# Kernel optimization log

Measured on AMD Instinct MI355X. Metric: run time of the kernel, lower is better.

## Reference

```python
import jax, jax.numpy as jnp
import numpy as np

N = 8192   # nodes per modality
D = 128    # hidden_channels
H = 2      # transformer heads
R = 15     # relations in HeteroConv (use_speaker='no')
E = 16384  # edges per relation
L = 2      # num_layers
# relation src/dst node-type ids: 0=audio, 1=text, 2=visual (dict order: a/v/t past, a/v/t future, a/v/t self, then cross)
SRC = np.array([0, 2, 1, 0, 2, 1, 0, 2, 1, 0, 0, 2, 2, 1, 1])
DST = np.array([0, 2, 1, 0, 2, 1, 0, 2, 1, 2, 1, 0, 1, 0, 2])


def setup_inputs() -> dict:
    key = jax.random.key(0)
    ks = jax.random.split(key, 18)
    f = lambda k, sh: jax.random.normal(k, sh, dtype=jnp.float32) * 0.05
    return {
        "x_audio": jax.random.normal(ks[0], (N, D), jnp.float32),
        "x_text": jax.random.normal(ks[1], (N, D), jnp.float32),
        "x_visual": jax.random.normal(ks[2], (N, D), jnp.float32),
        "edge_index": jax.random.randint(ks[3], (R, 2, E), 0, N, jnp.int32),
        "Wrel": f(ks[4], (L, R, D, D)),
        "brel": f(ks[5], (L, R, D)),
        "Wroot": f(ks[6], (L, R, D, D)),
        "Wq": f(ks[7], (D, H * D)), "bq": f(ks[8], (H * D,)),
        "Wk": f(ks[9], (D, H * D)), "bk": f(ks[10], (H * D,)),
        "Wv": f(ks[11], (D, H * D)), "bv": f(ks[12], (H * D,)),
        "Wskip": f(ks[13], (D, D)), "bskip": f(ks[14], (D,)),
        "gamma": jnp.ones((D,), jnp.float32),
        "beta": jnp.zeros((D,), jnp.float32),
    }


def reference(x_audio, x_text, x_visual, edge_index, Wrel, brel, Wroot,
              Wq, bq, Wk, bk, Wv, bv, Wskip, bskip, gamma, beta):
    src_t = jnp.asarray(SRC)
    dst_t = jnp.asarray(DST)
    x = jnp.stack([x_audio, x_text, x_visual])           # [3, N, D]
    src_idx = edge_index[:, 0]                            # [R, E]
    dst_idx = edge_index[:, 1]                            # [R, E]
    rel = jnp.arange(R)

    # --- HeteroConv of 15 GraphConvs (aggr='add' inside, 'mean' over the 5 relations per dst type) ---
    seg = (rel[:, None] * N + dst_idx).reshape(-1)        # per-relation segment ids
    for l in range(L):
        feats = jnp.take_along_axis(x[src_t], src_idx[:, :, None], axis=1)     # [R, E, D]
        msg = jax.ops.segment_sum(feats.reshape(R * E, D), seg,
                                  num_segments=R * N).reshape(R, N, D)          # scatter-add per relation
        out = (jnp.einsum('rnd,rde->rne', msg, Wrel[l]) + brel[l][:, None, :]
               + jnp.einsum('rnd,rde->rne', x[dst_t], Wroot[l]))                # lin_rel(agg) + lin_root(x_dst)
        x = jax.nn.relu(jnp.zeros_like(x).at[dst_t].add(out) / 5.0)            # mean over 5 relations per dst

    # --- hetero_to_homo: concat audio, text, visual (offsets 0, N, 2N) ---
    hx = x.reshape(3 * N, D)
    src_h = (src_t[:, None] * N + src_idx).reshape(-1)    # [R*E]
    dst_h = (dst_t[:, None] * N + dst_idx).reshape(-1)

    # --- TransformerConv (concat=False -> head mean, root skip) ---
    q = (hx @ Wq + bq).reshape(3 * N, H, D)
    k = (hx @ Wk + bk).reshape(3 * N, H, D)
    v = (hx @ Wv + bv).reshape(3 * N, H, D)
    logits = jnp.einsum('ehd,ehd->eh', q[dst_h], k[src_h]) / jnp.sqrt(jnp.float32(D))
    m = jax.ops.segment_max(logits, dst_h, num_segments=3 * N)
    p = jnp.exp(logits - m[dst_h])
    denom = jax.ops.segment_sum(p, dst_h, num_segments=3 * N)
    alpha = p / denom[dst_h]                              # segment softmax over incoming edges
    agg = jax.ops.segment_sum(alpha[:, :, None] * v[src_h], dst_h, num_segments=3 * N)  # [3N, H, D]
    out = agg.mean(axis=1) + hx @ Wskip + bskip

    # --- BatchNorm1d (training-mode batch stats) + leaky_relu ---
    mu = out.mean(axis=0)
    var = ((out - mu) ** 2).mean(axis=0)
    y = (out - mu) / jnp.sqrt(var + 1e-5) * gamma + beta
    y = jax.nn.leaky_relu(y)                              # negative_slope=0.01 (torch default)
    return y.reshape(3, N, D)                             # [audio, text, visual]
```

## Files before the change

### kernel.cpp

```cpp
#include <hip/hip_runtime.h>
#include <hip/hip_bf16.h>

#define NN 8192
#define DD 128
#define HH 2
#define RR 15
#define EE 16384
#define NLAYER 2
#define NMOD 3
#define TN (NMOD*NN)
#define NE (RR*EE)

#define SRC_BITS 0x16818618u
#define DST_BITS 0x21198618u
__device__ __forceinline__ int srcOf(int r) { return (SRC_BITS >> (2 * r)) & 3; }
__device__ __forceinline__ int dstOf(int r) { return (DST_BITS >> (2 * r)) & 3; }

typedef __attribute__((ext_vector_type(8))) short bf16x8;
typedef __attribute__((ext_vector_type(4))) float f32x4;

__device__ __forceinline__ unsigned short f2bf(float v) {
    union { float f; unsigned int u; } x; x.f = v;
    unsigned int r = (x.u + 0x7fffu + ((x.u >> 16) & 1u)) >> 16;
    return (unsigned short)r;
}
__device__ __forceinline__ float bf2f(unsigned int bits16) {
    return __uint_as_float(bits16 << 16);
}
__device__ __forceinline__ void bfu4(uint4 u, float* f) {
    f[0] = bf2f(u.x & 0xffffu); f[1] = bf2f(u.x >> 16);
    f[2] = bf2f(u.y & 0xffffu); f[3] = bf2f(u.y >> 16);
    f[4] = bf2f(u.z & 0xffffu); f[5] = bf2f(u.z >> 16);
    f[6] = bf2f(u.w & 0xffffu); f[7] = bf2f(u.w >> 16);
}

__global__ __launch_bounds__(256) void prep_all(
        const float* __restrict__ Wrel, const float* __restrict__ Wroot,
        const float* __restrict__ brel,
        const float* __restrict__ Wq, const float* __restrict__ Wk,
        const float* __restrict__ Wv, const float* __restrict__ Wskip,
        const float* __restrict__ xa, const float* __restrict__ xt,
        const float* __restrict__ xv,
        unsigned short* __restrict__ WrelT, unsigned short* __restrict__ WsumT,
        float* __restrict__ bsum,
        unsigned short* __restrict__ WqT, unsigned short* __restrict__ WkT,
        unsigned short* __restrict__ WvT, unsigned short* __restrict__ WskipT,
        unsigned short* __restrict__ xb, int* __restrict__ cnt) {
    int y = blockIdx.y;
    int t = blockIdx.x * 256 + threadIdx.x;
    if (y < 30) {
        int k = t >> 7, c = t & 127;
        WrelT[(size_t)y * 16384 + c * 128 + k] = f2bf(Wrel[(size_t)y * 16384 + t]);
    } else if (y < 36) {
        int mat = y - 30, l = mat / 3, m = mat % 3;
        int k = t >> 7, c = t & 127;
        float s = 0.f;
        #pragma unroll
        for (int r = 0; r < RR; r++)
            if (((DST_BITS >> (2 * r)) & 3) == (unsigned)m) s += Wroot[(size_t)(l * RR + r) * 16384 + t];
        WsumT[(size_t)mat * 16384 + c * 128 + k] = f2bf(s);
        if (blockIdx.x == 0 && threadIdx.x < 128) {
            float b = 0.f;
            #pragma unroll
            for (int r = 0; r < RR; r++)
                if (((DST_BITS >> (2 * r)) & 3) == (unsigned)m) b += brel[(l * RR + r) * 128 + threadIdx.x];
            bsum[mat * 128 + threadIdx.x] = b;
        }
    } else if (y < 39) {
        int which = y - 36;
        const float* s = which == 0 ? Wq : which == 1 ? Wk : Wv;
        unsigned short* d = which == 0 ? WqT : which == 1 ? WkT : WvT;
        #pragma unroll
        for (int it = 0; it < 2; it++) {
            int tt = t + it * 16384;
            int k = tt >> 8, c = tt & 255;
            d[c * 128 + k] = f2bf(s[tt]);
        }
    } else if (y == 39) {
        int k = t >> 7, c = t & 127;
        WskipT[c * 128 + k] = f2bf(Wskip[t]);
    } else if (y == 40) {
        for (int i = t; i < TN + 256; i += 16384) cnt[i] = 0;
    } else {
        int m = y - 41;
        const float* s = m == 0 ? xa : m == 1 ? xt : xv;
        unsigned short* d = xb + (size_t)m * NN * DD;
        for (int i = t * 4; i < NN * DD; i += 16384 * 4) {
            float4 v = *(const float4*)(s + i);
            uint2 o;
            o.x = (unsigned)f2bf(v.x) | ((unsigned)f2bf(v.y) << 16);
            o.y = (unsigned)f2bf(v.z) | ((unsigned)f2bf(v.w) << 16);
            *(uint2*)(d + i) = o;
        }
    }
}

__global__ void count_edges(const int* __restrict__ edge, int* __restrict__ cnt) {
    int t = blockIdx.x * 256 + threadIdx.x;
    if (t >= NE) return;
    int r = t >> 14, e = t & (EE - 1);
    int dst = edge[r * 2 * EE + EE + e];
    atomicAdd(&cnt[dstOf(r) * NN + dst], 1);
}

__global__ void scan_kernel(const int* __restrict__ cnt, int* __restrict__ startA,
                            int* __restrict__ cursor) {
    __shared__ int part[1024];
    int t = threadIdx.x;
    int base = t * (TN / 1024);
    int s = 0;
    for (int i = 0; i < TN / 1024; i++) s += cnt[base + i];
    part[t] = s;
    __syncthreads();
    for (int ofs = 1; ofs < 1024; ofs <<= 1) {
        int v = (t >= ofs) ? part[t - ofs] : 0;
        __syncthreads();
        part[t] += v;
        __syncthreads();
    }
    int run = (t == 0) ? 0 : part[t - 1];
    for (int i = 0; i < TN / 1024; i++) {
        startA[base + i] = run;
        cursor[base + i] = run;
        run += cnt[base + i];
    }
    if (t == 1023) startA[TN] = part[1023];
}

__global__ void place_edges(const int* __restrict__ edge, int* __restrict__ cursor,
                            unsigned int* __restrict__ sorted) {
    int t = blockIdx.x * 256 + threadIdx.x;
    if (t >= NE) return;
    int r = t >> 14, e = t & (EE - 1);
    int src = edge[r * 2 * EE + e];
    int dst = edge[r * 2 * EE + EE + e];
    int pos = atomicAdd(&cursor[dstOf(r) * NN + dst], 1);
    sorted[pos] = ((unsigned int)r << 13) | (unsigned int)src;
}

template<int MODE>
__device__ __forceinline__ void gemm_tile(const unsigned short* __restrict__ A,
                                          const unsigned short* __restrict__ BT,
                                          const float* __restrict__ bias,
                                          void* __restrict__ Cout,
                                          int ldc, int colofs, int row0,
                                          unsigned short* lds) {
    unsigned short* Alds = lds;
    unsigned short* Blds = lds + 16384;
    const int tid = threadIdx.x;
    const int lane = tid & 63;
    const int w = tid >> 6;
    #pragma unroll
    for (int i = 0; i < 8; i++) {
        int c = i * 256 + tid;
        int row = c >> 4;
        int k0 = (c & 15) << 3;
        uint4 va = *(const uint4*)(A + (size_t)(row0 + row) * 128 + k0);
        *(uint4*)((char*)Alds + (((row * 256 + k0 * 2)) ^ ((row & 7) << 4))) = va;
        uint4 vb = *(const uint4*)(BT + (size_t)row * 128 + k0);
        *(uint4*)((char*)Blds + (((row * 256 + k0 * 2)) ^ ((row & 7) << 4))) = vb;
    }
    __syncthreads();
    f32x4 acc[2][8];
    #pragma unroll
    for (int mi = 0; mi < 2; mi++)
        #pragma unroll
        for (int nj = 0; nj < 8; nj++) acc[mi][nj] = (f32x4){0.f, 0.f, 0.f, 0.f};
    const int lr = lane & 15, lk = lane >> 4;
    #pragma unroll
    for (int ks = 0; ks < 4; ks++) {
        bf16x8 a[2], b[8];
        #pragma unroll
        for (int mi = 0; mi < 2; mi++) {
            int row = w * 32 + mi * 16 + lr;
            a[mi] = *(const bf16x8*)((char*)Alds + ((row * 256 + (ks * 32 + lk * 8) * 2) ^ ((row & 7) << 4)));
        }
        #pragma unroll
        for (int nj = 0; nj < 8; nj++) {
            int row = nj * 16 + lr;
            b[nj] = *(const bf16x8*)((char*)Blds + ((row * 256 + (ks * 32 + lk * 8) * 2) ^ ((row & 7) << 4)));
        }
        #pragma unroll
        for (int mi = 0; mi < 2; mi++)
            #pragma unroll
            for (int nj = 0; nj < 8; nj++)
                acc[mi][nj] = __builtin_amdgcn_mfma_f32_16x16x32_bf16(a[mi], b[nj], acc[mi][nj], 0, 0, 0);
    }
    __syncthreads();
    float* Clds = (float*)lds;
    #pragma unroll
    for (int mi = 0; mi < 2; mi++) {
        #pragma unroll
        for (int nj = 0; nj < 8; nj++) {
            int ccl = nj * 16 + lr;
            float bb = bias ? bias[ccl] : 0.f;
            #pragma unroll
            for (int r = 0; r < 4; r++) {
                int row = w * 32 + mi * 16 + lk * 4 + r;
                Clds[row * 128 + ccl] = acc[mi][nj][r] + bb;
            }
        }
    }
    __syncthreads();
    #pragma unroll
    for (int p = 0; p < 8; p++) {
        int row = p * 16 + (tid >> 4);
        int c0 = (tid & 15) * 8;
        float4 fa = *(const float4*)(Clds + row * 128 + c0);
        float4 fb = *(const float4*)(Clds + row * 128 + c0 + 4);
        if (MODE == 2) {
            unsigned r0 = (unsigned)f2bf(fa.x) | ((unsigned)f2bf(fa.y) << 16);
            unsigned r1 = (unsigned)f2bf(fa.z) | ((unsigned)f2bf(fa.w) << 16);
            unsigned r2 = (unsigned)f2bf(fb.x) | ((unsigned)f2bf(fb.y) << 16);
            unsigned r3 = (unsigned)f2bf(fb.z) | ((unsigned)f2bf(fb.w) << 16);
            uint4 pk = {r0, r1, r2, r3};
            *(uint4*)((unsigned short*)Cout + (size_t)(row0 + row) * ldc + colofs + c0) = pk;
        } else {
            float* Cf = (float*)Cout;
            *(float4*)(Cf + (size_t)(row0 + row) * ldc + colofs + c0) = fa;
            *(float4*)(Cf + (size_t)(row0 + row) * ldc + colofs + c0 + 4) = fb;
        }
    }
}

__global__ __launch_bounds__(256) void zroot_gemm(const unsigned short* __restrict__ xbf,
                                                  const unsigned short* __restrict__ WrelT_l,
                                                  const unsigned short* __restrict__ WrootSumT_l,
                                                  const float* __restrict__ brelSum_l,
                                                  unsigned short* __restrict__ z,
                                                  unsigned short* __restrict__ xroot) {
    __shared__ unsigned short lds[2 * 16384];
    int y = blockIdx.y;
    if (y < RR) {
        gemm_tile<2>(xbf + (size_t)srcOf(y) * NN * 128, WrelT_l + (size_t)y * 16384, nullptr,
                     z + (size_t)y * NN * 128, 128, 0, blockIdx.x * 128, lds);
    } else {
        int m = y - RR;
        gemm_tile<2>(xbf + (size_t)m * NN * 128, WrootSumT_l + (size_t)m * 16384, brelSum_l + m * 128,
                     xroot + (size_t)m * NN * 128, 128, 0, blockIdx.x * 128, lds);
    }
}

__global__ __launch_bounds__(256) void qkvskip_gemm(const unsigned short* __restrict__ xbf,
                                                    const unsigned short* __restrict__ WqT,
                                                    const unsigned short* __restrict__ WkT,
                                                    const unsigned short* __restrict__ WvT,
                                                    const unsigned short* __restrict__ WskipT,
                                                    const float* __restrict__ bq,
                                                    const float* __restrict__ bk,
                                                    const float* __restrict__ bv,
                                                    const float* __restrict__ bskip,
                                                    unsigned short* __restrict__ qb,
                                                    unsigned short* __restrict__ kb,
                                                    unsigned short* __restrict__ vb,
                                                    float* __restrict__ out) {
    __shared__ unsigned short lds[2 * 16384];
    int y = blockIdx.y;
    if (y < 6) {
        int which = y >> 1, half = y & 1;
        const unsigned short* BT = (which == 0 ? WqT : which == 1 ? WkT : WvT) + half * 16384;
        const float* bias = (which == 0 ? bq : which == 1 ? bk : bv) + half * 128;
        unsigned short* C = (which == 0 ? qb : which == 1 ? kb : vb);
        gemm_tile<2>(xbf, BT, bias, C, 256, half * 128, blockIdx.x * 128, lds);
    } else {
        gemm_tile<0>(xbf, WskipT, bskip, out, 128, 0, blockIdx.x * 128, lds);
    }
}

__global__ __launch_bounds__(256) void gather_relu(const unsigned short* __restrict__ z,
                                                   const unsigned short* __restrict__ xroot,
                                                   const unsigned int* __restrict__ sorted,
                                                   const int* __restrict__ startA,
                                                   unsigned short* __restrict__ xout) {
    int node = blockIdx.x * 4 + (threadIdx.x >> 6);
    int lane = threadIdx.x & 63;
    int g = lane >> 4, p = lane & 15;
    int st = startA[node], en = startA[node + 1];
    float acc[8];
    #pragma unroll
    for (int j = 0; j < 8; j++) acc[j] = 0.f;
    int idx = st + g;
    unsigned int vcur = (idx < en) ? sorted[idx] : 0u;
    for (int base = st; base < en; base += 4) {
        unsigned int vnext = (idx + 4 < en) ? sorted[idx + 4] : 0u;
        uint4 u = *(const uint4*)(z + ((size_t)vcur << 7) + p * 8);
        if (idx < en) {
            float f[8]; bfu4(u, f);
            #pragma unroll
            for (int j = 0; j < 8; j++) acc[j] += f[j];
        }
        vcur = vnext;
        idx += 4;
    }
    #pragma unroll
    for (int j = 0; j < 8; j++) {
        acc[j] += __shfl_xor(acc[j], 32);
        acc[j] += __shfl_xor(acc[j], 16);
    }
    if (g == 0) {
        uint4 rt = *(const uint4*)(xroot + ((size_t)node << 7) + p * 8);
        float r[8]; bfu4(rt, r);
        unsigned short o[8];
        #pragma unroll
        for (int j = 0; j < 8; j++) {
            float v = (r[j] + acc[j]) * 0.2f;
            o[j] = f2bf(v > 0.f ? v : 0.f);
        }
        uint4 pk;
        pk.x = (unsigned)o[0] | ((unsigned)o[1] << 16);
        pk.y = (unsigned)o[2] | ((unsigned)o[3] << 16);
        pk.z = (unsigned)o[4] | ((unsigned)o[5] << 16);
        pk.w = (unsigned)o[6] | ((unsigned)o[7] << 16);
        *(uint4*)(xout + ((size_t)node << 7) + p * 8) = pk;
    }
}

__global__ __launch_bounds__(256) void attn_fused(const unsigned short* __restrict__ qb,
                                                  const unsigned short* __restrict__ kb,
                                                  const unsigned short* __restrict__ vb,
                                                  const unsigned int* __restrict__ sorted,
                                                  const int* __restrict__ startA,
                                                  float* __restrict__ out) {
    int node = blockIdx.x * 4 + (threadIdx.x >> 6);
    int lane = threadIdx.x & 63;
    int g = lane >> 4, p = lane & 15;
    float q0[8], q1[8];
    bfu4(*(const uint4*)(qb + (size_t)node * 256 + p * 8), q0);
    bfu4(*(const uint4*)(qb + (size_t)node * 256 + 128 + p * 8), q1);
    float m0 = -3.0e38f, m1 = -3.0e38f, s0 = 0.f, s1 = 0.f;
    float a0[8], a1[8];
    #pragma unroll
    for (int j = 0; j < 8; j++) { a0[j] = 0.f; a1[j] = 0.f; }
    int st = startA[node], en = startA[node + 1];
    int idx = st + g;
    unsigned int vcur = (idx < en) ? sorted[idx] : 0u;
    for (int base = st; base < en; base += 4) {
        unsigned int vnext = (idx + 4 < en) ? sorted[idx + 4] : 0u;
        bool valid = idx < en;
        int r = vcur >> 13;
        int srch = (int)(vcur & 8191u) + srcOf(r) * NN;
        const unsigned short* krow = kb + (size_t)srch * 256;
        const unsigned short* vrow = vb + (size_t)srch * 256;
        uint4 k0r = *(const uint4*)(krow + p * 8);
        uint4 k1r = *(const uint4*)(krow + 128 + p * 8);
        uint4 v0r = *(const uint4*)(vrow + p * 8);
        uint4 v1r = *(const uint4*)(vrow + 128 + p * 8);
        float k0[8], k1[8];
        bfu4(k0r, k0); bfu4(k1r, k1);
        float d0 = 0.f, d1 = 0.f;
        #pragma unroll
        for (int j = 0; j < 8; j++) { d0 += q0[j] * k0[j]; d1 += q1[j] * k1[j]; }
        #pragma unroll
        for (int off = 8; off >= 1; off >>= 1) {
            d0 += __shfl_xor(d0, off);
            d1 += __shfl_xor(d1, off);
        }
        float l0 = d0 * 0.08838834764831845f;
        float l1 = d1 * 0.08838834764831845f;
        float mn0 = fmaxf(m0, l0), mn1 = fmaxf(m1, l1);
        float sc0 = __expf(m0 - mn0), sc1 = __expf(m1 - mn1);
        float p0 = valid ? __expf(l0 - mn0) : 0.f;
        float p1 = valid ? __expf(l1 - mn1) : 0.f;
        s0 = s0 * sc0 + p0;
        s1 = s1 * sc1 + p1;
        float v0[8], v1[8];
        bfu4(v0r, v0); bfu4(v1r, v1);
        #pragma unroll
        for (int j = 0; j < 8; j++) {
            a0[j] = a0[j] * sc0 + p0 * v0[j];
            a1[j] = a1[j] * sc1 + p1 * v1[j];
        }
        m0 = mn0; m1 = mn1;
        vcur = vnext;
        idx += 4;
    }
    #pragma unroll
    for (int off = 32; off >= 16; off >>= 1) {
        float mo0 = __shfl_xor(m0, off), so0 = __shfl_xor(s0, off);
        float mo1 = __shfl_xor(m1, off), so1 = __shfl_xor(s1, off);
        float M0 = fmaxf(m0, mo0), M1 = fmaxf(m1, mo1);
        float e0 = __expf(m0 - M0), eo0 = __expf(mo0 - M0);
        float e1 = __expf(m1 - M1), eo1 = __expf(mo1 - M1);
        s0 = s0 * e0 + so0 * eo0;
        s1 = s1 * e1 + so1 * eo1;
        #pragma unroll
        for (int j = 0; j < 8; j++) {
            a0[j] = a0[j] * e0 + __shfl_xor(a0[j], off) * eo0;
            a1[j] = a1[j] * e1 + __shfl_xor(a1[j], off) * eo1;
        }
        m0 = M0; m1 = M1;
    }
    if (g == 0) {
        float inv0 = (s0 > 0.f) ? 0.5f / s0 : 0.f;
        float inv1 = (s1 > 0.f) ? 0.5f / s1 : 0.f;
        float* op = out + (size_t)node * 128 + p * 8;
        float4 ska = *(const float4*)op;
        float4 skb = *(const float4*)(op + 4);
        float4 ra, rb;
        ra.x = a0[0] * inv0 + a1[0] * inv1 + ska.x;
        ra.y = a0[1] * inv0 + a1[1] * inv1 + ska.y;
        ra.z = a0[2] * inv0 + a1[2] * inv1 + ska.z;
        ra.w = a0[3] * inv0 + a1[3] * inv1 + ska.w;
        rb.x = a0[4] * inv0 + a1[4] * inv1 + skb.x;
        rb.y = a0[5] * inv0 + a1[5] * inv1 + skb.y;
        rb.z = a0[6] * inv0 + a1[6] * inv1 + skb.z;
        rb.w = a0[7] * inv0 + a1[7] * inv1 + skb.w;
        *(float4*)op = ra;
        *(float4*)(op + 4) = rb;
    }
}

__global__ void colstats(const float* __restrict__ outb, float* __restrict__ stats) {
    int col = threadIdx.x & 127;
    int sub = threadIdx.x >> 7;
    float s = 0.f, ss = 0.f;
    for (int row = blockIdx.x * 2 + sub; row < TN; row += gridDim.x * 2) {
        float vv = outb[(size_t)row * DD + col];
        s += vv;
        ss += vv * vv;
    }
    __shared__ float red[2][256];
    red[0][threadIdx.x] = s;
    red[1][threadIdx.x] = ss;
    __syncthreads();
    if (sub == 0) {
        s  += red[0][threadIdx.x + 128];
        ss += red[1][threadIdx.x + 128];
        atomicAdd(&stats[col], s);
        atomicAdd(&stats[DD + col], ss);
    }
}

__global__ void ln_act(float* __restrict__ outb, const float* __restrict__ stats,
                       const float* __restrict__ gamma, const float* __restrict__ beta) {
    int i = (blockIdx.x * 256 + threadIdx.x) * 4;
    if (i >= TN * DD) return;
    int col = i & 127;
    float4 v = *(const float4*)(outb + i);
    float o[4] = {v.x, v.y, v.z, v.w};
    #pragma unroll
    for (int j = 0; j < 4; j++) {
        int c = col + j;
        float mu = stats[c] * (1.f / TN);
        float var = stats[DD + c] * (1.f / TN) - mu * mu;
        float inv = rsqrtf(var + 1e-5f);
        float vv = (o[j] - mu) * inv * gamma[c] + beta[c];
        o[j] = vv > 0.f ? vv : 0.01f * vv;
    }
    float4 res = {o[0], o[1], o[2], o[3]};
    *(float4*)(outb + i) = res;
}

extern "C" void kernel_launch(void* const* d_in, const int* in_sizes, int n_in,
                              void* d_out, int out_size, void* d_ws, size_t ws_size,
                              hipStream_t stream) {
    const float* x_audio = (const float*)d_in[0];
    const float* x_text  = (const float*)d_in[1];
    const float* x_vis   = (const float*)d_in[2];
    const int*   edge    = (const int*)d_in[3];
    const float* Wrel    = (const float*)d_in[4];
    const float* brel    = (const float*)d_in[5];
    const float* Wroot   = (const float*)d_in[6];
    const float* Wq      = (const float*)d_in[7];
    const float* bq      = (const float*)d_in[8];
    const float* Wk      = (const float*)d_in[9];
    const float* bk      = (const float*)d_in[10];
    const float* Wv      = (const float*)d_in[11];
    const float* bv      = (const float*)d_in[12];
    const float* Wskip   = (const float*)d_in[13];
    const float* bskip   = (const float*)d_in[14];
    const float* gamma   = (const float*)d_in[15];
    const float* beta    = (const float*)d_in[16];
    float* out = (float*)d_out;

    char* p = (char*)d_ws;
    unsigned short* xbfA = (unsigned short*)p; p += (size_t)TN * 128 * 2;
    unsigned short* xbfB = (unsigned short*)p; p += (size_t)TN * 128 * 2;
    unsigned short* zqkv = (unsigned short*)p; p += (size_t)3 * TN * 256 * 2;
    unsigned short* z  = zqkv;
    unsigned short* qb = zqkv;
    unsigned short* kb = zqkv + (size_t)TN * 256;
    unsigned short* vb = zqkv + (size_t)2 * TN * 256;
    unsigned short* xroot = (unsigned short*)p; p += (size_t)TN * 128 * 2;
    unsigned short* WrelT = (unsigned short*)p; p += (size_t)2 * RR * 16384 * 2;
    unsigned short* WrootSumT = (unsigned short*)p; p += (size_t)6 * 16384 * 2;
    float* brelSum = (float*)p; p += 6 * 128 * 4;
    unsigned short* WqT = (unsigned short*)p; p += 256 * 128 * 2;
    unsigned short* WkT = (unsigned short*)p; p += 256 * 128 * 2;
    unsigned short* WvT = (unsigned short*)p; p += 256 * 128 * 2;
    unsigned short* WskipT = (unsigned short*)p; p += 128 * 128 * 2;
    unsigned int* sorted = (unsigned int*)p; p += (size_t)NE * 4;
    int* startA = (int*)p; p += (TN + 1) * 4;
    int* cursor = (int*)p; p += (TN + 1) * 4;
    int* cnt = (int*)p; p += TN * 4;
    float* stats = (float*)p; p += 256 * 4;
    size_t needed = (size_t)(p - (char*)d_ws);
    if (ws_size < needed) return;

    prep_all<<<dim3(64, 44), 256, 0, stream>>>(Wrel, Wroot, brel, Wq, Wk, Wv, Wskip,
                                               x_audio, x_text, x_vis,
                                               WrelT, WrootSumT, brelSum,
                                               WqT, WkT, WvT, WskipT, xbfA, cnt);

    count_edges<<<NE / 256, 256, 0, stream>>>(edge, cnt);
    scan_kernel<<<1, 1024, 0, stream>>>(cnt, startA, cursor);
    place_edges<<<NE / 256, 256, 0, stream>>>(edge, cursor, sorted);

    unsigned short* xcur = xbfA;
    unsigned short* xnxt = xbfB;
    for (int l = 0; l < NLAYER; ++l) {
        zroot_gemm<<<dim3(NN / 128, RR + NMOD), 256, 0, stream>>>(
            xcur, WrelT + (size_t)l * RR * 16384, WrootSumT + (size_t)l * NMOD * 16384,
            brelSum + l * NMOD * 128, z, xroot);
        gather_relu<<<TN / 4, 256, 0, stream>>>(z, xroot, sorted, startA, xnxt);
        unsigned short* t = xcur; xcur = xnxt; xnxt = t;
    }

    qkvskip_gemm<<<dim3(TN / 128, 7), 256, 0, stream>>>(xcur, WqT, WkT, WvT, WskipT,
                                                        bq, bk, bv, bskip, qb, kb, vb, out);
    attn_fused<<<TN / 4, 256, 0, stream>>>(qb, kb, vb, sorted, startA, out);

    colstats<<<96, 256, 0, stream>>>(out, stats);
    ln_act<<<(TN * DD) / 1024, 256, 0, stream>>>(out, stats, gamma, beta);
}
```

Before: 222.6 us.

## Drop online-softmax max, use fp16 dot2 for QK, prepack source index

```diff
diff --git a/kernel.cpp b/kernel.cpp
--- a/kernel.cpp
+++ b/kernel.cpp
@@ -18,6 +18,7 @@
 
 typedef __attribute__((ext_vector_type(8))) short bf16x8;
 typedef __attribute__((ext_vector_type(4))) float f32x4;
+typedef _Float16 h2 __attribute__((ext_vector_type(2)));
 
 __device__ __forceinline__ unsigned short f2bf(float v) {
     union { float f; unsigned int u; } x; x.f = v;
@@ -32,6 +33,26 @@
     f[2] = bf2f(u.y & 0xffffu); f[3] = bf2f(u.y >> 16);
     f[4] = bf2f(u.z & 0xffffu); f[5] = bf2f(u.z >> 16);
     f[6] = bf2f(u.w & 0xffffu); f[7] = bf2f(u.w >> 16);
+}
+
+__device__ __forceinline__ float dot8_f16(uint4 a, uint4 b, float acc) {
+#if __has_builtin(__builtin_amdgcn_fdot2)
+    acc = __builtin_amdgcn_fdot2(__builtin_bit_cast(h2, a.x), __builtin_bit_cast(h2, b.x), acc, false);
+    acc = __builtin_amdgcn_fdot2(__builtin_bit_cast(h2, a.y), __builtin_bit_cast(h2, b.y), acc, false);
+    acc = __builtin_amdgcn_fdot2(__builtin_bit_cast(h2, a.z), __builtin_bit_cast(h2, b.z), acc, false);
+    acc = __builtin_amdgcn_fdot2(__builtin_bit_cast(h2, a.w), __builtin_bit_cast(h2, b.w), acc, false);
+#else
+    h2 av, bv;
+    av = __builtin_bit_cast(h2, a.x); bv = __builtin_bit_cast(h2, b.x);
+    acc += (float)av.x * (float)bv.x + (float)av.y * (float)bv.y;
+    av = __builtin_bit_cast(h2, a.y); bv = __builtin_bit_cast(h2, b.y);
+    acc += (float)av.x * (float)bv.x + (float)av.y * (float)bv.y;
+    av = __builtin_bit_cast(h2, a.z); bv = __builtin_bit_cast(h2, b.z);
+    acc += (float)av.x * (float)bv.x + (float)av.y * (float)bv.y;
+    av = __builtin_bit_cast(h2, a.w); bv = __builtin_bit_cast(h2, b.w);
+    acc += (float)av.x * (float)bv.x + (float)av.y * (float)bv.y;
+#endif
+    return acc;
 }
 
 __global__ __launch_bounds__(256) void prep_all(
@@ -135,7 +156,9 @@
     int src = edge[r * 2 * EE + e];
     int dst = edge[r * 2 * EE + EE + e];
     int pos = atomicAdd(&cursor[dstOf(r) * NN + dst], 1);
-    sorted[pos] = ((unsigned int)r << 13) | (unsigned int)src;
+    unsigned int zrow = ((unsigned int)r << 13) | (unsigned int)src;
+    unsigned int srch = (unsigned int)(srcOf(r) * NN + src);
+    sorted[pos] = (zrow << 15) | srch;
 }
 
 template<int MODE>
@@ -144,7 +167,7 @@
                                           const float* __restrict__ bias,
                                           void* __restrict__ Cout,
                                           int ldc, int colofs, int row0,
-                                          unsigned short* lds) {
+                                          unsigned short* lds, float oscale = 1.f) {
     unsigned short* Alds = lds;
     unsigned short* Blds = lds + 16384;
     const int tid = threadIdx.x;
@@ -213,6 +236,13 @@
             unsigned r1 = (unsigned)f2bf(fa.z) | ((unsigned)f2bf(fa.w) << 16);
             unsigned r2 = (unsigned)f2bf(fb.x) | ((unsigned)f2bf(fb.y) << 16);
             unsigned r3 = (unsigned)f2bf(fb.z) | ((unsigned)f2bf(fb.w) << 16);
+            uint4 pk = {r0, r1, r2, r3};
+            *(uint4*)((unsigned short*)Cout + (size_t)(row0 + row) * ldc + colofs + c0) = pk;
+        } else if (MODE == 3) {
+            unsigned r0 = __builtin_bit_cast(unsigned, __builtin_amdgcn_cvt_pkrtz(fa.x * oscale, fa.y * oscale));
+            unsigned r1 = __builtin_bit_cast(unsigned, __builtin_amdgcn_cvt_pkrtz(fa.z * oscale, fa.w * oscale));
+            unsigned r2 = __builtin_bit_cast(unsigned, __builtin_amdgcn_cvt_pkrtz(fb.x * oscale, fb.y * oscale));
+            unsigned r3 = __builtin_bit_cast(unsigned, __builtin_amdgcn_cvt_pkrtz(fb.z * oscale, fb.w * oscale));
             uint4 pk = {r0, r1, r2, r3};
             *(uint4*)((unsigned short*)Cout + (size_t)(row0 + row) * ldc + colofs + c0) = pk;
         } else {
@@ -256,12 +286,16 @@
                                                     float* __restrict__ out) {
     __shared__ unsigned short lds[2 * 16384];
     int y = blockIdx.y;
-    if (y < 6) {
+    if (y < 4) {
         int which = y >> 1, half = y & 1;
-        const unsigned short* BT = (which == 0 ? WqT : which == 1 ? WkT : WvT) + half * 16384;
-        const float* bias = (which == 0 ? bq : which == 1 ? bk : bv) + half * 128;
-        unsigned short* C = (which == 0 ? qb : which == 1 ? kb : vb);
-        gemm_tile<2>(xbf, BT, bias, C, 256, half * 128, blockIdx.x * 128, lds);
+        const unsigned short* BT = (which == 0 ? WqT : WkT) + half * 16384;
+        const float* bias = (which == 0 ? bq : bk) + half * 128;
+        unsigned short* C = (which == 0 ? qb : kb);
+        float os = (which == 0) ? 0.08838834764831845f : 1.f;
+        gemm_tile<3>(xbf, BT, bias, C, 256, half * 128, blockIdx.x * 128, lds, os);
+    } else if (y < 6) {
+        int half = y & 1;
+        gemm_tile<2>(xbf, WvT + half * 16384, bv + half * 128, vb, 256, half * 128, blockIdx.x * 128, lds);
     } else {
         gemm_tile<0>(xbf, WskipT, bskip, out, 128, 0, blockIdx.x * 128, lds);
     }
@@ -283,7 +317,7 @@
     unsigned int vcur = (idx < en) ? sorted[idx] : 0u;
     for (int base = st; base < en; base += 4) {
         unsigned int vnext = (idx + 4 < en) ? sorted[idx + 4] : 0u;
-        uint4 u = *(const uint4*)(z + ((size_t)vcur << 7) + p * 8);
+        uint4 u = *(const uint4*)(z + ((size_t)(vcur >> 15) << 7) + p * 8);
         if (idx < en) {
             float f[8]; bfu4(u, f);
             #pragma unroll
@@ -324,10 +358,9 @@
     int node = blockIdx.x * 4 + (threadIdx.x >> 6);
     int lane = threadIdx.x & 63;
     int g = lane >> 4, p = lane & 15;
-    float q0[8], q1[8];
-    bfu4(*(const uint4*)(qb + (size_t)node * 256 + p * 8), q0);
-    bfu4(*(const uint4*)(qb + (size_t)node * 256 + 128 + p * 8), q1);
-    float m0 = -3.0e38f, m1 = -3.0e38f, s0 = 0.f, s1 = 0.f;
+    uint4 q0 = *(const uint4*)(qb + (size_t)node * 256 + p * 8);
+    uint4 q1 = *(const uint4*)(qb + (size_t)node * 256 + 128 + p * 8);
+    float s0 = 0.f, s1 = 0.f;
     float a0[8], a1[8];
     #pragma unroll
     for (int j = 0; j < 8; j++) { a0[j] = 0.f; a1[j] = 0.f; }
@@ -337,58 +370,42 @@
     for (int base = st; base < en; base += 4) {
         unsigned int vnext = (idx + 4 < en) ? sorted[idx + 4] : 0u;
         bool valid = idx < en;
-        int r = vcur >> 13;
-        int srch = (int)(vcur & 8191u) + srcOf(r) * NN;
+        int srch = (int)(vcur & 32767u);
         const unsigned short* krow = kb + (size_t)srch * 256;
         const unsigned short* vrow = vb + (size_t)srch * 256;
         uint4 k0r = *(const uint4*)(krow + p * 8);
         uint4 k1r = *(const uint4*)(krow + 128 + p * 8);
         uint4 v0r = *(const uint4*)(vrow + p * 8);
         uint4 v1r = *(const uint4*)(vrow + 128 + p * 8);
-        float k0[8], k1[8];
-        bfu4(k0r, k0); bfu4(k1r, k1);
-        float d0 = 0.f, d1 = 0.f;
-        #pragma unroll
-        for (int j = 0; j < 8; j++) { d0 += q0[j] * k0[j]; d1 += q1[j] * k1[j]; }
+        float d0 = dot8_f16(q0, k0r, 0.f);
+        float d1 = dot8_f16(q1, k1r, 0.f);
         #pragma unroll
         for (int off = 8; off >= 1; off >>= 1) {
             d0 += __shfl_xor(d0, off);
             d1 += __shfl_xor(d1, off);
         }
-        float l0 = d0 * 0.08838834764831845f;
-        float l1 = d1 * 0.08838834764831845f;
-        float mn0 = fmaxf(m0, l0), mn1 = fmaxf(m1, l1);
-        float sc0 = __expf(m0 - mn0), sc1 = __expf(m1 - mn1);
-        float p0 = valid ? __expf(l0 - mn0) : 0.f;
-        float p1 = valid ? __expf(l1 - mn1) : 0.f;
-        s0 = s0 * sc0 + p0;
-        s1 = s1 * sc1 + p1;
+        float p0 = valid ? __expf(d0) : 0.f;
+        float p1 = valid ? __expf(d1) : 0.f;
+        s0 += p0; s1 += p1;
         float v0[8], v1[8];
         bfu4(v0r, v0); bfu4(v1r, v1);
         #pragma unroll
         for (int j = 0; j < 8; j++) {
-            a0[j] = a0[j] * sc0 + p0 * v0[j];
-            a1[j] = a1[j] * sc1 + p1 * v1[j];
-        }
-        m0 = mn0; m1 = mn1;
+            a0[j] += p0 * v0[j];
+            a1[j] += p1 * v1[j];
+        }
         vcur = vnext;
         idx += 4;
     }
     #pragma unroll
     for (int off = 32; off >= 16; off >>= 1) {
-        float mo0 = __shfl_xor(m0, off), so0 = __shfl_xor(s0, off);
-        float mo1 = __shfl_xor(m1, off), so1 = __shfl_xor(s1, off);
-        float M0 = fmaxf(m0, mo0), M1 = fmaxf(m1, mo1);
-        float e0 = __expf(m0 - M0), eo0 = __expf(mo0 - M0);
-        float e1 = __expf(m1 - M1), eo1 = __expf(mo1 - M1);
-        s0 = s0 * e0 + so0 * eo0;
-        s1 = s1 * e1 + so1 * eo1;
+        s0 += __shfl_xor(s0, off);
+        s1 += __shfl_xor(s1, off);
         #pragma unroll
         for (int j = 0; j < 8; j++) {
-            a0[j] = a0[j] * e0 + __shfl_xor(a0[j], off) * eo0;
-            a1[j] = a1[j] * e1 + __shfl_xor(a1[j], off) * eo1;
-        }
-        m0 = M0; m1 = M1;
+            a0[j] += __shfl_xor(a0[j], off);
+            a1[j] += __shfl_xor(a1[j], off);
+        }
     }
     if (g == 0) {
         float inv0 = (s0 > 0.f) ? 0.5f / s0 : 0.f;
@@ -520,6 +537,6 @@
                                                         bq, bk, bv, bskip, qb, kb, vb, out);
     attn_fused<<<TN / 4, 256, 0, stream>>>(qb, kb, vb, sorted, startA, out);
 
-    colstats<<<96, 256, 0, stream>>>(out, stats);
+    colstats<<<384, 256, 0, stream>>>(out, stats);
     ln_act<<<(TN * DD) / 1024, 256, 0, stream>>>(out, stats, gamma, beta);
 }
```

Result: faster. 207.2 us (-7.0%).
